# Kernel optimization log

Measured on AMD Instinct MI355X. Metric: run time of the kernel, lower is better.

The kernel has to match this reference:

```python
import jax, jax.numpy as jnp
import numpy as np

B, T, C = 8, 1024, 768
H = 12
HS = C // H  # 64


def setup_inputs() -> dict:
    key = jax.random.key(0)
    ks = jax.random.split(key, 6)
    s = C ** -0.5
    x = jax.random.normal(ks[0], (B, T, C), dtype=jnp.float32)
    Wq = jax.random.normal(ks[1], (H, C, HS), dtype=jnp.float32) * s
    Wk = jax.random.normal(ks[2], (H, C, HS), dtype=jnp.float32) * s
    Wv = jax.random.normal(ks[3], (H, C, HS), dtype=jnp.float32) * s
    Wproj = jax.random.normal(ks[4], (C, C), dtype=jnp.float32) * s
    bproj = jax.random.normal(ks[5], (C,), dtype=jnp.float32) * 0.01
    return {"x": x, "Wq": Wq, "Wk": Wk, "Wv": Wv, "Wproj": Wproj, "bproj": bproj}


def reference(x, Wq, Wk, Wv, Wproj, bproj):
    # per-head projections (equivalent to stacked per-head nn.Linear, bias=False)
    q = jnp.einsum('btc,hcd->bhtd', x, Wq)
    k = jnp.einsum('btc,hcd->bhtd', x, Wk)
    v = jnp.einsum('btc,hcd->bhtd', x, Wv)
    scale = HS ** -0.5
    scores = jnp.einsum('bhtd,bhsd->bhts', q, k) * scale  # [B,H,T,T]
    causal = jnp.tril(jnp.ones((T, T), dtype=bool))
    scores = jnp.where(causal, scores, -jnp.inf)
    weights = jax.nn.softmax(scores, axis=-1)
    out = jnp.einsum('bhts,bhsd->bhtd', weights, v)  # [B,H,T,HS]
    out = out.transpose(0, 2, 1, 3).reshape(B, T, C)  # concat heads
    # output projection (dropout is identity in eval mode)
    return out @ Wproj.T + bproj
```

## Files before the change

kernel.cpp:

```cpp
#include <hip/hip_runtime.h>


typedef short bf16x8 __attribute__((ext_vector_type(8)));
typedef float f32x4 __attribute__((ext_vector_type(4)));

static __device__ __forceinline__ unsigned short f2bf(float f) {
  unsigned int u = __float_as_uint(f);
  u += 0x7fffu + ((u >> 16) & 1u);
  return (unsigned short)(u >> 16);
}

static __device__ __forceinline__ void gl_lds16(const void* g, void* l) {
  __builtin_amdgcn_global_load_lds(
      (const __attribute__((address_space(1))) unsigned int*)g,
      (__attribute__((address_space(3))) unsigned int*)l, 16, 0, 0);
}

__global__ void k_cast4(const float* __restrict__ src, unsigned short* __restrict__ dst, int n4) {
  int i = blockIdx.x * 256 + threadIdx.x;
  if (i < n4) {
    float4 f = ((const float4*)src)[i];
    ushort4 o;
    o.x = f2bf(f.x); o.y = f2bf(f.y); o.z = f2bf(f.z); o.w = f2bf(f.w);
    ((ushort4*)dst)[i] = o;
  }
}

__global__ __launch_bounds__(256) void k_prep_w(const float* __restrict__ Wq,
                                                const float* __restrict__ Wk,
                                                const float* __restrict__ Wv,
                                                unsigned short* __restrict__ wt) {
  __shared__ float tb[64][65];
  const int c0 = blockIdx.x * 64;
  const int hq = blockIdx.y;
  const int qi = hq / 12, h = hq % 12;
  const float* W = (qi == 0) ? Wq : ((qi == 1) ? Wk : Wv);
  const int tid = threadIdx.x;
  {
    int rowb = tid >> 4;
    int col4 = (tid & 15) * 4;
#pragma unroll
    for (int it = 0; it < 4; ++it) {
      int c = it * 16 + rowb;
      float4 f = *(const float4*)(W + (h * 768 + c0 + c) * 64 + col4);
      tb[c][col4] = f.x; tb[c][col4 + 1] = f.y; tb[c][col4 + 2] = f.z; tb[c][col4 + 3] = f.w;
    }
  }
  __syncthreads();
#pragma unroll
  for (int it = 0; it < 2; ++it) {
    int slot = it * 256 + tid;
    int d = slot >> 3, cg = (slot & 7) * 8;
    union { unsigned short a[8]; uint4 v; } o;
#pragma unroll
    for (int j = 0; j < 8; ++j) o.a[j] = f2bf(tb[cg + j][d]);
    *(uint4*)(wt + (qi * 768 + h * 64 + d) * 768 + c0 + cg) = o.v;
  }
}

__global__ __launch_bounds__(256) void k_gemm_qkv(
    const unsigned short* __restrict__ xb,
    const unsigned short* __restrict__ wt,
    unsigned short* __restrict__ qkv) {
  __shared__ unsigned short As[128 * 32];
  __shared__ unsigned short Bs[128 * 32];
  const int tid = threadIdx.x;
  const int w = tid >> 6, lane = tid & 63, quad = lane >> 4, lr = lane & 15;
  const int wm = w >> 1, wn = w & 1;
  const int m0 = blockIdx.x * 128, n0 = blockIdx.y * 128;

  f32x4 acc[4][4] = {};

  const int srow = w * 16 + (lane >> 2);
  const int scol = (lane & 3) * 8;
  const unsigned short* ga0 = xb + (m0 + srow) * 768 + scol;
  const unsigned short* ga1 = ga0 + 64 * 768;
  const unsigned short* gb0 = wt + (n0 + srow) * 768 + scol;
  const unsigned short* gb1 = gb0 + 64 * 768;
  unsigned short* la0 = &As[(w * 16) * 32];
  unsigned short* la1 = la0 + 64 * 32;
  unsigned short* lb0 = &Bs[(w * 16) * 32];
  unsigned short* lb1 = lb0 + 64 * 32;

  for (int k0 = 0; k0 < 768; k0 += 32) {
    gl_lds16(ga0 + k0, la0);
    gl_lds16(ga1 + k0, la1);
    gl_lds16(gb0 + k0, lb0);
    gl_lds16(gb1 + k0, lb1);
    __syncthreads();
    bf16x8 af[4], bfr[4];
#pragma unroll
    for (int i = 0; i < 4; ++i)
      af[i] = *(const bf16x8*)(&As[(wm * 64 + i * 16 + lr) * 32 + quad * 8]);
#pragma unroll
    for (int j = 0; j < 4; ++j)
      bfr[j] = *(const bf16x8*)(&Bs[(wn * 64 + j * 16 + lr) * 32 + quad * 8]);
#pragma unroll
    for (int i = 0; i < 4; ++i)
#pragma unroll
      for (int j = 0; j < 4; ++j)
        acc[i][j] = __builtin_amdgcn_mfma_f32_16x16x32_bf16(af[i], bfr[j], acc[i][j], 0, 0, 0);
    __syncthreads();
  }

#pragma unroll
  for (int j = 0; j < 4; ++j) {
    int n = n0 + wn * 64 + j * 16 + lr;
    int qi = n / 768;
    int rr = n - qi * 768;
    int h = rr >> 6, d = rr & 63;
#pragma unroll
    for (int i = 0; i < 4; ++i) {
#pragma unroll
      for (int r = 0; r < 4; ++r) {
        int m = m0 + wm * 64 + i * 16 + quad * 4 + r;
        int b = m >> 10, t = m & 1023;
        qkv[(((qi * 8 + b) * 12 + h) * 1024 + t) * 64 + d] = f2bf(acc[i][j][r]);
      }
    }
  }
}

__global__ __launch_bounds__(256) void k_transV(const unsigned short* __restrict__ Vn,
                                                unsigned short* __restrict__ Vt) {
  __shared__ unsigned short tb[64][80];
  const int t0 = blockIdx.x * 64;
  const int bh = blockIdx.y;
  const unsigned short* src = Vn + bh * 65536;
  unsigned short* dst = Vt + bh * 65536;
  const int tid = threadIdx.x;
#pragma unroll
  for (int p = 0; p < 2; ++p) {
    int idx = p * 256 + tid;
    int row = idx >> 3, c8 = idx & 7;
    *(uint4*)&tb[row][c8 * 8] = *(const uint4*)(src + (t0 + row) * 64 + c8 * 8);
  }
  __syncthreads();
  int d = tid >> 2, tq = (tid & 3) * 16;
  unsigned short tmp[16];
#pragma unroll
  for (int k = 0; k < 16; ++k) tmp[k] = tb[tq + k][d];
  *(uint4*)(dst + d * 1024 + t0 + tq) = *(uint4*)&tmp[0];
  *(uint4*)(dst + d * 1024 + t0 + tq + 8) = *(uint4*)&tmp[8];
}

__global__ __launch_bounds__(256) void k_attn(
    const unsigned short* __restrict__ qkv,
    const unsigned short* __restrict__ Vtg,
    unsigned short* __restrict__ attn) {
  __shared__ unsigned short Kbuf[2][64 * 64];
  __shared__ unsigned short Vbuf[2][64 * 64];
  __shared__ unsigned short Pbuf[4][32 * 72];
  const int tid = threadIdx.x;
  const int w = tid >> 6, lane = tid & 63, quad = lane >> 4, lr = lane & 15;
  const int hb = blockIdx.x;
  const int qb = 7 - (int)blockIdx.y;
  const int h = hb % 12, b = hb / 12;
  const int HT = 65536;
  const unsigned short* Q  = qkv + (b * 12 + h) * HT;
  const unsigned short* K  = qkv + (96 + b * 12 + h) * HT;
  const unsigned short* Vt = Vtg + (b * 12 + h) * HT;

  bf16x8 aq[2][2];
#pragma unroll
  for (int i = 0; i < 2; ++i)
#pragma unroll
    for (int hf = 0; hf < 2; ++hf)
      aq[i][hf] = *(const bf16x8*)(Q + (qb * 128 + w * 32 + i * 16 + lr) * 64 + hf * 32 + quad * 8);

  f32x4 accO[2][4] = {};
  float lsum[2][4] = {};

  const int nc = 2 * qb + 2;
  const float c1 = 0.125f * 1.4426950408889634f;
  const float c0 = -4.0f * 1.4426950408889634f;

  auto stage = [&](int bi, int sc) {
#pragma unroll
    for (int j = 0; j < 2; ++j) {
      int row = w * 16 + j * 8 + (lane >> 3);
      int c8 = (lane & 7) ^ (row & 7);
      gl_lds16(K + (sc * 64 + row) * 64 + c8 * 8, &Kbuf[bi][(w * 16 + j * 8) * 64]);
      gl_lds16(Vt + row * 1024 + sc * 64 + c8 * 8, &Vbuf[bi][(w * 16 + j * 8) * 64]);
    }
  };

  stage(0, 0);
  for (int sc = 0; sc < nc; ++sc) {
    __syncthreads();
    if (sc + 1 < nc) stage((sc + 1) & 1, sc + 1);
    const unsigned short* Kl = Kbuf[sc & 1];
    const unsigned short* Vl = Vbuf[sc & 1];

    f32x4 accS[2][4];
#pragma unroll
    for (int i = 0; i < 2; ++i)
#pragma unroll
      for (int nt = 0; nt < 4; ++nt) {
        f32x4 z = {};
#pragma unroll
        for (int hf = 0; hf < 2; ++hf) {
          int s = nt * 16 + lr;
          bf16x8 kb = *(const bf16x8*)(Kl + (s * 8 + ((4 * hf + quad) ^ (s & 7))) * 8);
          z = __builtin_amdgcn_mfma_f32_16x16x32_bf16(aq[i][hf], kb, z, 0, 0, 0);
        }
        accS[i][nt] = z;
      }

#pragma unroll
    for (int i = 0; i < 2; ++i) {
      const int base_i = qb * 128 + w * 32 + i * 16;
      const bool needmask = (sc * 64 + 63 > base_i);
#pragma unroll
      for (int r = 0; r < 4; ++r) {
        int tg = base_i + quad * 4 + r;
#pragma unroll
        for (int nt = 0; nt < 4; ++nt) {
          float p = __builtin_amdgcn_exp2f(fmaf(accS[i][nt][r], c1, c0));
          if (needmask && (sc * 64 + nt * 16 + lr > tg)) p = 0.f;
          lsum[i][r] += p;
          Pbuf[w][(i * 16 + quad * 4 + r) * 72 + nt * 16 + lr] = f2bf(p);
        }
      }
    }

#pragma unroll
    for (int i = 0; i < 2; ++i) {
      bf16x8 pa[2];
#pragma unroll
      for (int hf = 0; hf < 2; ++hf)
        pa[hf] = *(const bf16x8*)(&Pbuf[w][(i * 16 + lr) * 72 + hf * 32 + quad * 8]);
#pragma unroll
      for (int ntd = 0; ntd < 4; ++ntd) {
        int d = ntd * 16 + lr;
#pragma unroll
        for (int hf = 0; hf < 2; ++hf) {
          bf16x8 vb = *(const bf16x8*)(Vl + (d * 8 + ((4 * hf + quad) ^ (d & 7))) * 8);
          accO[i][ntd] = __builtin_amdgcn_mfma_f32_16x16x32_bf16(pa[hf], vb, accO[i][ntd], 0, 0, 0);
        }
      }
    }
  }

  float linv[2][4];
#pragma unroll
  for (int i = 0; i < 2; ++i)
#pragma unroll
    for (int r = 0; r < 4; ++r) {
      float l = lsum[i][r];
      l += __shfl_xor(l, 1);
      l += __shfl_xor(l, 2);
      l += __shfl_xor(l, 4);
      l += __shfl_xor(l, 8);
      linv[i][r] = 1.0f / l;
    }

#pragma unroll
  for (int i = 0; i < 2; ++i)
#pragma unroll
    for (int ntd = 0; ntd < 4; ++ntd) {
      int c = h * 64 + ntd * 16 + lr;
#pragma unroll
      for (int r = 0; r < 4; ++r) {
        int t = qb * 128 + w * 32 + i * 16 + quad * 4 + r;
        attn[(b * 1024 + t) * 768 + c] = f2bf(accO[i][ntd][r] * linv[i][r]);
      }
    }
}

__global__ __launch_bounds__(256) void k_gemm_proj(
    const unsigned short* __restrict__ ab,
    const unsigned short* __restrict__ wp,
    const float* __restrict__ bias,
    float* __restrict__ out) {
  __shared__ unsigned short As[128 * 32];
  __shared__ unsigned short Bs[128 * 32];
  const int tid = threadIdx.x;
  const int w = tid >> 6, lane = tid & 63, quad = lane >> 4, lr = lane & 15;
  const int wm = w >> 1, wn = w & 1;
  const int m0 = blockIdx.x * 128, n0 = blockIdx.y * 128;

  f32x4 acc[4][4] = {};

  const int srow = w * 16 + (lane >> 2);
  const int scol = (lane & 3) * 8;
  const unsigned short* ga0 = ab + (m0 + srow) * 768 + scol;
  const unsigned short* ga1 = ga0 + 64 * 768;
  const unsigned short* gb0 = wp + (n0 + srow) * 768 + scol;
  const unsigned short* gb1 = gb0 + 64 * 768;
  unsigned short* la0 = &As[(w * 16) * 32];
  unsigned short* la1 = la0 + 64 * 32;
  unsigned short* lb0 = &Bs[(w * 16) * 32];
  unsigned short* lb1 = lb0 + 64 * 32;

  for (int k0 = 0; k0 < 768; k0 += 32) {
    gl_lds16(ga0 + k0, la0);
    gl_lds16(ga1 + k0, la1);
    gl_lds16(gb0 + k0, lb0);
    gl_lds16(gb1 + k0, lb1);
    __syncthreads();
    bf16x8 af[4], bfr[4];
#pragma unroll
    for (int i = 0; i < 4; ++i)
      af[i] = *(const bf16x8*)(&As[(wm * 64 + i * 16 + lr) * 32 + quad * 8]);
#pragma unroll
    for (int j = 0; j < 4; ++j)
      bfr[j] = *(const bf16x8*)(&Bs[(wn * 64 + j * 16 + lr) * 32 + quad * 8]);
#pragma unroll
    for (int i = 0; i < 4; ++i)
#pragma unroll
      for (int j = 0; j < 4; ++j)
        acc[i][j] = __builtin_amdgcn_mfma_f32_16x16x32_bf16(af[i], bfr[j], acc[i][j], 0, 0, 0);
    __syncthreads();
  }

#pragma unroll
  for (int j = 0; j < 4; ++j) {
    int ncol = n0 + wn * 64 + j * 16 + lr;
    float bv = bias[ncol];
#pragma unroll
    for (int i = 0; i < 4; ++i) {
#pragma unroll
      for (int r = 0; r < 4; ++r) {
        int m = m0 + wm * 64 + i * 16 + quad * 4 + r;
        out[m * 768 + ncol] = acc[i][j][r] + bv;
      }
    }
  }
}

extern "C" void kernel_launch(void* const* d_in, const int* in_sizes, int n_in,
                              void* d_out, int out_size, void* d_ws, size_t ws_size,
                              hipStream_t stream) {
  const float* x     = (const float*)d_in[0];
  const float* Wq    = (const float*)d_in[1];
  const float* Wk    = (const float*)d_in[2];
  const float* Wv    = (const float*)d_in[3];
  const float* Wproj = (const float*)d_in[4];
  const float* bproj = (const float*)d_in[5];
  float* out = (float*)d_out;

  char* p = (char*)d_ws;
  unsigned short* xb   = (unsigned short*)p; p += 12582912;
  unsigned short* wt   = (unsigned short*)p; p += 3538944;
  unsigned short* wp   = (unsigned short*)p; p += 1179648;
  unsigned short* qkv  = (unsigned short*)p; p += 37748736;
  unsigned short* attn = (unsigned short*)p; p += 12582912;
  unsigned short* Vt   = xb;
  const unsigned short* Vn = qkv + 2 * 96 * 65536;

  k_cast4<<<6144, 256, 0, stream>>>(x, xb, 8192 * 768 / 4);
  k_cast4<<<576, 256, 0, stream>>>(Wproj, wp, 768 * 768 / 4);
  k_prep_w<<<dim3(12, 36), 256, 0, stream>>>(Wq, Wk, Wv, wt);
  k_gemm_qkv<<<dim3(64, 18), 256, 0, stream>>>(xb, wt, qkv);
  k_transV<<<dim3(16, 96), 256, 0, stream>>>(Vn, Vt);
  k_attn<<<dim3(96, 8), 256, 0, stream>>>(qkv, Vt, attn);
  k_gemm_proj<<<dim3(64, 6), 256, 0, stream>>>(attn, wp, bproj, out);
}
```

Baseline: 196.7 us.

## Fuse prep kernels, write V transposed from QKV GEMM, stage epilogues through LDS

The three cast/prep launches are merged into a single kernel indexed by block id. The QKV GEMM now stages its output tile in shared memory and writes Q/K rows, and V already transposed, with 16-byte stores, which removes the separate V transpose kernel and its extra global round trip. The projection GEMM epilogue also goes through LDS so that bias add and fp32 stores become coalesced float4 writes. The cost is extra LDS traffic and barriers in the epilogues, plus higher LDS use from the union buffers.

```diff
diff --git a/kernel.cpp b/kernel.cpp
--- a/kernel.cpp
+++ b/kernel.cpp
@@ -16,26 +16,30 @@
       (__attribute__((address_space(3))) unsigned int*)l, 16, 0, 0);
 }
 
-__global__ void k_cast4(const float* __restrict__ src, unsigned short* __restrict__ dst, int n4) {
-  int i = blockIdx.x * 256 + threadIdx.x;
-  if (i < n4) {
+__global__ __launch_bounds__(256) void k_prep(
+    const float* __restrict__ x, const float* __restrict__ Wproj,
+    const float* __restrict__ Wq, const float* __restrict__ Wk,
+    const float* __restrict__ Wv,
+    unsigned short* __restrict__ xb, unsigned short* __restrict__ wp,
+    unsigned short* __restrict__ wt) {
+  __shared__ float tb[64][65];
+  const int bx = blockIdx.x;
+  const int tid = threadIdx.x;
+  if (bx < 6720) {
+    const float* src = (bx < 6144) ? x : Wproj;
+    unsigned short* dst = (bx < 6144) ? xb : wp;
+    int i = (bx < 6144 ? bx : bx - 6144) * 256 + tid;
     float4 f = ((const float4*)src)[i];
     ushort4 o;
     o.x = f2bf(f.x); o.y = f2bf(f.y); o.z = f2bf(f.z); o.w = f2bf(f.w);
     ((ushort4*)dst)[i] = o;
-  }
-}
-
-__global__ __launch_bounds__(256) void k_prep_w(const float* __restrict__ Wq,
-                                                const float* __restrict__ Wk,
-                                                const float* __restrict__ Wv,
-                                                unsigned short* __restrict__ wt) {
-  __shared__ float tb[64][65];
-  const int c0 = blockIdx.x * 64;
-  const int hq = blockIdx.y;
+    return;
+  }
+  const int idx = bx - 6720;
+  const int c0 = (idx % 12) * 64;
+  const int hq = idx / 12;
   const int qi = hq / 12, h = hq % 12;
   const float* W = (qi == 0) ? Wq : ((qi == 1) ? Wk : Wv);
-  const int tid = threadIdx.x;
   {
     int rowb = tid >> 4;
     int col4 = (tid & 15) * 4;
@@ -61,9 +65,12 @@
 __global__ __launch_bounds__(256) void k_gemm_qkv(
     const unsigned short* __restrict__ xb,
     const unsigned short* __restrict__ wt,
-    unsigned short* __restrict__ qkv) {
-  __shared__ unsigned short As[128 * 32];
-  __shared__ unsigned short Bs[128 * 32];
+    unsigned short* __restrict__ qkv,
+    unsigned short* __restrict__ vt) {
+  __shared__ union {
+    unsigned short ab[2][128 * 32];
+    unsigned short c[128][132];
+  } sm;
   const int tid = threadIdx.x;
   const int w = tid >> 6, lane = tid & 63, quad = lane >> 4, lr = lane & 15;
   const int wm = w >> 1, wn = w & 1;
@@ -77,9 +84,11 @@
   const unsigned short* ga1 = ga0 + 64 * 768;
   const unsigned short* gb0 = wt + (n0 + srow) * 768 + scol;
   const unsigned short* gb1 = gb0 + 64 * 768;
-  unsigned short* la0 = &As[(w * 16) * 32];
+  unsigned short* As = sm.ab[0];
+  unsigned short* Bs = sm.ab[1];
+  unsigned short* la0 = As + (w * 16) * 32;
   unsigned short* la1 = la0 + 64 * 32;
-  unsigned short* lb0 = &Bs[(w * 16) * 32];
+  unsigned short* lb0 = Bs + (w * 16) * 32;
   unsigned short* lb1 = lb0 + 64 * 32;
 
   for (int k0 = 0; k0 < 768; k0 += 32) {
@@ -104,44 +113,36 @@
   }
 
 #pragma unroll
-  for (int j = 0; j < 4; ++j) {
-    int n = n0 + wn * 64 + j * 16 + lr;
-    int qi = n / 768;
-    int rr = n - qi * 768;
-    int h = rr >> 6, d = rr & 63;
-#pragma unroll
-    for (int i = 0; i < 4; ++i) {
-#pragma unroll
-      for (int r = 0; r < 4; ++r) {
-        int m = m0 + wm * 64 + i * 16 + quad * 4 + r;
-        int b = m >> 10, t = m & 1023;
-        qkv[(((qi * 8 + b) * 12 + h) * 1024 + t) * 64 + d] = f2bf(acc[i][j][r]);
-      }
-    }
-  }
-}
-
-__global__ __launch_bounds__(256) void k_transV(const unsigned short* __restrict__ Vn,
-                                                unsigned short* __restrict__ Vt) {
-  __shared__ unsigned short tb[64][80];
-  const int t0 = blockIdx.x * 64;
-  const int bh = blockIdx.y;
-  const unsigned short* src = Vn + bh * 65536;
-  unsigned short* dst = Vt + bh * 65536;
-  const int tid = threadIdx.x;
-#pragma unroll
-  for (int p = 0; p < 2; ++p) {
-    int idx = p * 256 + tid;
-    int row = idx >> 3, c8 = idx & 7;
-    *(uint4*)&tb[row][c8 * 8] = *(const uint4*)(src + (t0 + row) * 64 + c8 * 8);
-  }
+  for (int i = 0; i < 4; ++i)
+#pragma unroll
+    for (int j = 0; j < 4; ++j)
+#pragma unroll
+      for (int r = 0; r < 4; ++r)
+        sm.c[wm * 64 + i * 16 + quad * 4 + r][wn * 64 + j * 16 + lr] = f2bf(acc[i][j][r]);
   __syncthreads();
-  int d = tid >> 2, tq = (tid & 3) * 16;
-  unsigned short tmp[16];
-#pragma unroll
-  for (int k = 0; k < 16; ++k) tmp[k] = tb[tq + k][d];
-  *(uint4*)(dst + d * 1024 + t0 + tq) = *(uint4*)&tmp[0];
-  *(uint4*)(dst + d * 1024 + t0 + tq + 8) = *(uint4*)&tmp[8];
+
+  const int qi = n0 / 768;
+  const int rr0 = n0 - qi * 768;
+  const int h0 = rr0 >> 6;
+  const int b = m0 >> 10, t0 = m0 & 1023;
+  if (qi < 2) {
+    int t_local = tid >> 1, hh = tid & 1;
+    unsigned short* dst = qkv + (size_t)(((qi * 8 + b) * 12 + h0 + hh) * 1024 + t0 + t_local) * 64;
+    const unsigned short* src = &sm.c[t_local][hh * 64];
+#pragma unroll
+    for (int k = 0; k < 8; ++k)
+      *(uint4*)(dst + k * 8) = *(const uint4*)(src + k * 8);
+  } else {
+    int hh = tid >> 7, d = (tid >> 1) & 63, th = tid & 1;
+    unsigned short* dst = vt + (size_t)((b * 12 + h0 + hh) * 64 + d) * 1024 + t0 + th * 64;
+#pragma unroll
+    for (int k0 = 0; k0 < 8; ++k0) {
+      union { unsigned short a[8]; uint4 v; } o;
+#pragma unroll
+      for (int kk = 0; kk < 8; ++kk) o.a[kk] = sm.c[th * 64 + k0 * 8 + kk][hh * 64 + d];
+      *(uint4*)(dst + k0 * 8) = o.v;
+    }
+  }
 }
 
 __global__ __launch_bounds__(256) void k_attn(
@@ -273,8 +274,10 @@
     const unsigned short* __restrict__ wp,
     const float* __restrict__ bias,
     float* __restrict__ out) {
-  __shared__ unsigned short As[128 * 32];
-  __shared__ unsigned short Bs[128 * 32];
+  __shared__ union {
+    unsigned short ab2[2][128 * 32];
+    float cf[64][134];
+  } sm;
   const int tid = threadIdx.x;
   const int w = tid >> 6, lane = tid & 63, quad = lane >> 4, lr = lane & 15;
   const int wm = w >> 1, wn = w & 1;
@@ -288,9 +291,11 @@
   const unsigned short* ga1 = ga0 + 64 * 768;
   const unsigned short* gb0 = wp + (n0 + srow) * 768 + scol;
   const unsigned short* gb1 = gb0 + 64 * 768;
-  unsigned short* la0 = &As[(w * 16) * 32];
+  unsigned short* As = sm.ab2[0];
+  unsigned short* Bs = sm.ab2[1];
+  unsigned short* la0 = As + (w * 16) * 32;
   unsigned short* la1 = la0 + 64 * 32;
-  unsigned short* lb0 = &Bs[(w * 16) * 32];
+  unsigned short* lb0 = Bs + (w * 16) * 32;
   unsigned short* lb1 = lb0 + 64 * 32;
 
   for (int k0 = 0; k0 < 768; k0 += 32) {
@@ -315,17 +320,28 @@
   }
 
 #pragma unroll
-  for (int j = 0; j < 4; ++j) {
-    int ncol = n0 + wn * 64 + j * 16 + lr;
-    float bv = bias[ncol];
-#pragma unroll
-    for (int i = 0; i < 4; ++i) {
-#pragma unroll
-      for (int r = 0; r < 4; ++r) {
-        int m = m0 + wm * 64 + i * 16 + quad * 4 + r;
-        out[m * 768 + ncol] = acc[i][j][r] + bv;
-      }
-    }
+  for (int p = 0; p < 2; ++p) {
+    if (wm == p) {
+#pragma unroll
+      for (int i = 0; i < 4; ++i)
+#pragma unroll
+        for (int j = 0; j < 4; ++j)
+#pragma unroll
+          for (int r = 0; r < 4; ++r)
+            sm.cf[i * 16 + quad * 4 + r][wn * 64 + j * 16 + lr] = acc[i][j][r];
+    }
+    __syncthreads();
+    int row = tid >> 2, cq = (tid & 3) * 32;
+    const float* brow = bias + n0 + cq;
+    float* orow = out + (size_t)(m0 + p * 64 + row) * 768 + n0 + cq;
+#pragma unroll
+    for (int k = 0; k < 8; ++k) {
+      float4 v = *(const float4*)&sm.cf[row][cq + k * 4];
+      float4 bv = *(const float4*)(brow + k * 4);
+      v.x += bv.x; v.y += bv.y; v.z += bv.z; v.w += bv.w;
+      *(float4*)(orow + k * 4) = v;
+    }
+    __syncthreads();
   }
 }
 
@@ -346,14 +362,10 @@
   unsigned short* wp   = (unsigned short*)p; p += 1179648;
   unsigned short* qkv  = (unsigned short*)p; p += 37748736;
   unsigned short* attn = (unsigned short*)p; p += 12582912;
-  unsigned short* Vt   = xb;
-  const unsigned short* Vn = qkv + 2 * 96 * 65536;
-
-  k_cast4<<<6144, 256, 0, stream>>>(x, xb, 8192 * 768 / 4);
-  k_cast4<<<576, 256, 0, stream>>>(Wproj, wp, 768 * 768 / 4);
-  k_prep_w<<<dim3(12, 36), 256, 0, stream>>>(Wq, Wk, Wv, wt);
-  k_gemm_qkv<<<dim3(64, 18), 256, 0, stream>>>(xb, wt, qkv);
-  k_transV<<<dim3(16, 96), 256, 0, stream>>>(Vn, Vt);
-  k_attn<<<dim3(96, 8), 256, 0, stream>>>(qkv, Vt, attn);
+  unsigned short* vt   = qkv + (size_t)192 * 65536;
+
+  k_prep<<<7152, 256, 0, stream>>>(x, Wproj, Wq, Wk, Wv, xb, wp, wt);
+  k_gemm_qkv<<<dim3(64, 18), 256, 0, stream>>>(xb, wt, qkv, vt);
+  k_attn<<<dim3(96, 8), 256, 0, stream>>>(qkv, vt, attn);
   k_gemm_proj<<<dim3(64, 6), 256, 0, stream>>>(attn, wp, bproj, out);
 }
```

After: 203.3 us. 3.3% more time.

## Merge prep kernels, pad Pbuf differently, stage proj epilogue through LDS

Applied to the files above, without the earlier changes.

Folds the two cast launches and the weight-transpose launch into a single prep kernel that dispatches on block index, so two kernel launches are removed. The padding of the attention P buffer's row stride changes from 72 to 68 elements to alter the LDS bank mapping. The output-projection epilogue now stages accumulators through shared memory (unioned with the A/B tiles) in two halves and writes coalesced float4 rows with the bias added, replacing scattered scalar stores at the cost of extra barriers and LDS traffic.

```diff
diff --git a/kernel.cpp b/kernel.cpp
--- a/kernel.cpp
+++ b/kernel.cpp
@@ -16,26 +16,30 @@
       (__attribute__((address_space(3))) unsigned int*)l, 16, 0, 0);
 }
 
-__global__ void k_cast4(const float* __restrict__ src, unsigned short* __restrict__ dst, int n4) {
-  int i = blockIdx.x * 256 + threadIdx.x;
-  if (i < n4) {
+__global__ __launch_bounds__(256) void k_prep(
+    const float* __restrict__ x, const float* __restrict__ Wproj,
+    const float* __restrict__ Wq, const float* __restrict__ Wk,
+    const float* __restrict__ Wv,
+    unsigned short* __restrict__ xb, unsigned short* __restrict__ wp,
+    unsigned short* __restrict__ wt) {
+  __shared__ float tb[64][65];
+  const int bx = blockIdx.x;
+  const int tid = threadIdx.x;
+  if (bx < 6720) {
+    const float* src = (bx < 6144) ? x : Wproj;
+    unsigned short* dst = (bx < 6144) ? xb : wp;
+    int i = (bx < 6144 ? bx : bx - 6144) * 256 + tid;
     float4 f = ((const float4*)src)[i];
     ushort4 o;
     o.x = f2bf(f.x); o.y = f2bf(f.y); o.z = f2bf(f.z); o.w = f2bf(f.w);
     ((ushort4*)dst)[i] = o;
-  }
-}
-
-__global__ __launch_bounds__(256) void k_prep_w(const float* __restrict__ Wq,
-                                                const float* __restrict__ Wk,
-                                                const float* __restrict__ Wv,
-                                                unsigned short* __restrict__ wt) {
-  __shared__ float tb[64][65];
-  const int c0 = blockIdx.x * 64;
-  const int hq = blockIdx.y;
+    return;
+  }
+  const int idx = bx - 6720;
+  const int c0 = (idx % 12) * 64;
+  const int hq = idx / 12;
   const int qi = hq / 12, h = hq % 12;
   const float* W = (qi == 0) ? Wq : ((qi == 1) ? Wk : Wv);
-  const int tid = threadIdx.x;
   {
     int rowb = tid >> 4;
     int col4 = (tid & 15) * 4;
@@ -150,7 +154,7 @@
     unsigned short* __restrict__ attn) {
   __shared__ unsigned short Kbuf[2][64 * 64];
   __shared__ unsigned short Vbuf[2][64 * 64];
-  __shared__ unsigned short Pbuf[4][32 * 72];
+  __shared__ unsigned short Pbuf[4][32 * 68];
   const int tid = threadIdx.x;
   const int w = tid >> 6, lane = tid & 63, quad = lane >> 4, lr = lane & 15;
   const int hb = blockIdx.x;
@@ -219,7 +223,7 @@
           float p = __builtin_amdgcn_exp2f(fmaf(accS[i][nt][r], c1, c0));
           if (needmask && (sc * 64 + nt * 16 + lr > tg)) p = 0.f;
           lsum[i][r] += p;
-          Pbuf[w][(i * 16 + quad * 4 + r) * 72 + nt * 16 + lr] = f2bf(p);
+          Pbuf[w][(i * 16 + quad * 4 + r) * 68 + nt * 16 + lr] = f2bf(p);
         }
       }
     }
@@ -229,7 +233,7 @@
       bf16x8 pa[2];
 #pragma unroll
       for (int hf = 0; hf < 2; ++hf)
-        pa[hf] = *(const bf16x8*)(&Pbuf[w][(i * 16 + lr) * 72 + hf * 32 + quad * 8]);
+        pa[hf] = *(const bf16x8*)(&Pbuf[w][(i * 16 + lr) * 68 + hf * 32 + quad * 8]);
 #pragma unroll
       for (int ntd = 0; ntd < 4; ++ntd) {
         int d = ntd * 16 + lr;
@@ -273,8 +277,10 @@
     const unsigned short* __restrict__ wp,
     const float* __restrict__ bias,
     float* __restrict__ out) {
-  __shared__ unsigned short As[128 * 32];
-  __shared__ unsigned short Bs[128 * 32];
+  __shared__ union {
+    unsigned short ab2[2][128 * 32];
+    float cf[64][134];
+  } sm;
   const int tid = threadIdx.x;
   const int w = tid >> 6, lane = tid & 63, quad = lane >> 4, lr = lane & 15;
   const int wm = w >> 1, wn = w & 1;
@@ -288,9 +294,11 @@
   const unsigned short* ga1 = ga0 + 64 * 768;
   const unsigned short* gb0 = wp + (n0 + srow) * 768 + scol;
   const unsigned short* gb1 = gb0 + 64 * 768;
-  unsigned short* la0 = &As[(w * 16) * 32];
+  unsigned short* As = sm.ab2[0];
+  unsigned short* Bs = sm.ab2[1];
+  unsigned short* la0 = As + (w * 16) * 32;
   unsigned short* la1 = la0 + 64 * 32;
-  unsigned short* lb0 = &Bs[(w * 16) * 32];
+  unsigned short* lb0 = Bs + (w * 16) * 32;
   unsigned short* lb1 = lb0 + 64 * 32;
 
   for (int k0 = 0; k0 < 768; k0 += 32) {
@@ -315,17 +323,28 @@
   }
 
 #pragma unroll
-  for (int j = 0; j < 4; ++j) {
-    int ncol = n0 + wn * 64 + j * 16 + lr;
-    float bv = bias[ncol];
-#pragma unroll
-    for (int i = 0; i < 4; ++i) {
-#pragma unroll
-      for (int r = 0; r < 4; ++r) {
-        int m = m0 + wm * 64 + i * 16 + quad * 4 + r;
-        out[m * 768 + ncol] = acc[i][j][r] + bv;
-      }
-    }
+  for (int p = 0; p < 2; ++p) {
+    if (wm == p) {
+#pragma unroll
+      for (int i = 0; i < 4; ++i)
+#pragma unroll
+        for (int j = 0; j < 4; ++j)
+#pragma unroll
+          for (int r = 0; r < 4; ++r)
+            sm.cf[i * 16 + quad * 4 + r][wn * 64 + j * 16 + lr] = acc[i][j][r];
+    }
+    __syncthreads();
+    int row = tid >> 2, cq = (tid & 3) * 32;
+    const float* brow = bias + n0 + cq;
+    float* orow = out + (size_t)(m0 + p * 64 + row) * 768 + n0 + cq;
+#pragma unroll
+    for (int k = 0; k < 8; ++k) {
+      float4 v = *(const float4*)&sm.cf[row][cq + k * 4];
+      float4 bv = *(const float4*)(brow + k * 4);
+      v.x += bv.x; v.y += bv.y; v.z += bv.z; v.w += bv.w;
+      *(float4*)(orow + k * 4) = v;
+    }
+    __syncthreads();
   }
 }
 
@@ -347,11 +366,9 @@
   unsigned short* qkv  = (unsigned short*)p; p += 37748736;
   unsigned short* attn = (unsigned short*)p; p += 12582912;
   unsigned short* Vt   = xb;
-  const unsigned short* Vn = qkv + 2 * 96 * 65536;
-
-  k_cast4<<<6144, 256, 0, stream>>>(x, xb, 8192 * 768 / 4);
-  k_cast4<<<576, 256, 0, stream>>>(Wproj, wp, 768 * 768 / 4);
-  k_prep_w<<<dim3(12, 36), 256, 0, stream>>>(Wq, Wk, Wv, wt);
+  const unsigned short* Vn = qkv + (size_t)192 * 65536;
+
+  k_prep<<<7152, 256, 0, stream>>>(x, Wproj, Wq, Wk, Wv, xb, wp, wt);
   k_gemm_qkv<<<dim3(64, 18), 256, 0, stream>>>(xb, wt, qkv);
   k_transV<<<dim3(16, 96), 256, 0, stream>>>(Vn, Vt);
   k_attn<<<dim3(96, 8), 256, 0, stream>>>(qkv, Vt, attn);
```

New measurement: 204.4 us. 3.9% more time.

## Fuse prep kernels and write V transposed directly from QKV GEMM epilogue

Applied to the files above, without the earlier changes.

Merges the x cast, Wproj cast and QKV weight transpose into one launch with block-index dispatch. The QKV GEMM epilogue now writes V straight into a transposed [b,h,d,t] layout with 8-byte stores, so the separate V transpose kernel and its extra read/write pass over V are gone. The attention P buffer row stride is also changed from 72 to 68 to alter LDS bank mapping. Risks include less coalesced V stores and possible bank or alignment effects from the new P stride.

```diff
diff --git a/kernel.cpp b/kernel.cpp
--- a/kernel.cpp
+++ b/kernel.cpp
@@ -16,26 +16,30 @@
       (__attribute__((address_space(3))) unsigned int*)l, 16, 0, 0);
 }
 
-__global__ void k_cast4(const float* __restrict__ src, unsigned short* __restrict__ dst, int n4) {
-  int i = blockIdx.x * 256 + threadIdx.x;
-  if (i < n4) {
+__global__ __launch_bounds__(256) void k_prep(
+    const float* __restrict__ x, const float* __restrict__ Wproj,
+    const float* __restrict__ Wq, const float* __restrict__ Wk,
+    const float* __restrict__ Wv,
+    unsigned short* __restrict__ xb, unsigned short* __restrict__ wp,
+    unsigned short* __restrict__ wt) {
+  __shared__ float tb[64][65];
+  const int bx = blockIdx.x;
+  const int tid = threadIdx.x;
+  if (bx < 6720) {
+    const float* src = (bx < 6144) ? x : Wproj;
+    unsigned short* dst = (bx < 6144) ? xb : wp;
+    int i = (bx < 6144 ? bx : bx - 6144) * 256 + tid;
     float4 f = ((const float4*)src)[i];
     ushort4 o;
     o.x = f2bf(f.x); o.y = f2bf(f.y); o.z = f2bf(f.z); o.w = f2bf(f.w);
     ((ushort4*)dst)[i] = o;
-  }
-}
-
-__global__ __launch_bounds__(256) void k_prep_w(const float* __restrict__ Wq,
-                                                const float* __restrict__ Wk,
-                                                const float* __restrict__ Wv,
-                                                unsigned short* __restrict__ wt) {
-  __shared__ float tb[64][65];
-  const int c0 = blockIdx.x * 64;
-  const int hq = blockIdx.y;
+    return;
+  }
+  const int idx = bx - 6720;
+  const int c0 = (idx % 12) * 64;
+  const int hq = idx / 12;
   const int qi = hq / 12, h = hq % 12;
   const float* W = (qi == 0) ? Wq : ((qi == 1) ? Wk : Wv);
-  const int tid = threadIdx.x;
   {
     int rowb = tid >> 4;
     int col4 = (tid & 15) * 4;
@@ -61,7 +65,8 @@
 __global__ __launch_bounds__(256) void k_gemm_qkv(
     const unsigned short* __restrict__ xb,
     const unsigned short* __restrict__ wt,
-    unsigned short* __restrict__ qkv) {
+    unsigned short* __restrict__ qkv,
+    unsigned short* __restrict__ vt) {
   __shared__ unsigned short As[128 * 32];
   __shared__ unsigned short Bs[128 * 32];
   const int tid = threadIdx.x;
@@ -103,45 +108,38 @@
     __syncthreads();
   }
 
-#pragma unroll
-  for (int j = 0; j < 4; ++j) {
-    int n = n0 + wn * 64 + j * 16 + lr;
-    int qi = n / 768;
-    int rr = n - qi * 768;
-    int h = rr >> 6, d = rr & 63;
-#pragma unroll
-    for (int i = 0; i < 4; ++i) {
-#pragma unroll
-      for (int r = 0; r < 4; ++r) {
-        int m = m0 + wm * 64 + i * 16 + quad * 4 + r;
-        int b = m >> 10, t = m & 1023;
-        qkv[(((qi * 8 + b) * 12 + h) * 1024 + t) * 64 + d] = f2bf(acc[i][j][r]);
-      }
-    }
-  }
-}
-
-__global__ __launch_bounds__(256) void k_transV(const unsigned short* __restrict__ Vn,
-                                                unsigned short* __restrict__ Vt) {
-  __shared__ unsigned short tb[64][80];
-  const int t0 = blockIdx.x * 64;
-  const int bh = blockIdx.y;
-  const unsigned short* src = Vn + bh * 65536;
-  unsigned short* dst = Vt + bh * 65536;
-  const int tid = threadIdx.x;
-#pragma unroll
-  for (int p = 0; p < 2; ++p) {
-    int idx = p * 256 + tid;
-    int row = idx >> 3, c8 = idx & 7;
-    *(uint4*)&tb[row][c8 * 8] = *(const uint4*)(src + (t0 + row) * 64 + c8 * 8);
-  }
-  __syncthreads();
-  int d = tid >> 2, tq = (tid & 3) * 16;
-  unsigned short tmp[16];
-#pragma unroll
-  for (int k = 0; k < 16; ++k) tmp[k] = tb[tq + k][d];
-  *(uint4*)(dst + d * 1024 + t0 + tq) = *(uint4*)&tmp[0];
-  *(uint4*)(dst + d * 1024 + t0 + tq + 8) = *(uint4*)&tmp[8];
+  const int qi = n0 / 768;
+  const int b = m0 >> 10, t0 = m0 & 1023;
+  if (qi < 2) {
+#pragma unroll
+    for (int j = 0; j < 4; ++j) {
+      int rr = (n0 - qi * 768) + wn * 64 + j * 16 + lr;
+      int h = rr >> 6, d = rr & 63;
+#pragma unroll
+      for (int i = 0; i < 4; ++i) {
+#pragma unroll
+        for (int r = 0; r < 4; ++r) {
+          int t = t0 + wm * 64 + i * 16 + quad * 4 + r;
+          qkv[(size_t)(((qi * 8 + b) * 12 + h) * 1024 + t) * 64 + d] = f2bf(acc[i][j][r]);
+        }
+      }
+    }
+  } else {
+#pragma unroll
+    for (int j = 0; j < 4; ++j) {
+      int rr = (n0 - 1536) + wn * 64 + j * 16 + lr;
+      int h = rr >> 6, d = rr & 63;
+      unsigned short* vrow = vt + (size_t)((b * 12 + h) * 64 + d) * 1024;
+#pragma unroll
+      for (int i = 0; i < 4; ++i) {
+        int t = t0 + wm * 64 + i * 16 + quad * 4;
+        union { unsigned short a[4]; unsigned int u[2]; } o;
+#pragma unroll
+        for (int r = 0; r < 4; ++r) o.a[r] = f2bf(acc[i][j][r]);
+        *(uint2*)(vrow + t) = *(uint2*)&o.u[0];
+      }
+    }
+  }
 }
 
 __global__ __launch_bounds__(256) void k_attn(
@@ -150,7 +148,7 @@
     unsigned short* __restrict__ attn) {
   __shared__ unsigned short Kbuf[2][64 * 64];
   __shared__ unsigned short Vbuf[2][64 * 64];
-  __shared__ unsigned short Pbuf[4][32 * 72];
+  __shared__ unsigned short Pbuf[4][32 * 68];
   const int tid = threadIdx.x;
   const int w = tid >> 6, lane = tid & 63, quad = lane >> 4, lr = lane & 15;
   const int hb = blockIdx.x;
@@ -219,7 +217,7 @@
           float p = __builtin_amdgcn_exp2f(fmaf(accS[i][nt][r], c1, c0));
           if (needmask && (sc * 64 + nt * 16 + lr > tg)) p = 0.f;
           lsum[i][r] += p;
-          Pbuf[w][(i * 16 + quad * 4 + r) * 72 + nt * 16 + lr] = f2bf(p);
+          Pbuf[w][(i * 16 + quad * 4 + r) * 68 + nt * 16 + lr] = f2bf(p);
         }
       }
     }
@@ -229,7 +227,7 @@
       bf16x8 pa[2];
 #pragma unroll
       for (int hf = 0; hf < 2; ++hf)
-        pa[hf] = *(const bf16x8*)(&Pbuf[w][(i * 16 + lr) * 72 + hf * 32 + quad * 8]);
+        pa[hf] = *(const bf16x8*)(&Pbuf[w][(i * 16 + lr) * 68 + hf * 32 + quad * 8]);
 #pragma unroll
       for (int ntd = 0; ntd < 4; ++ntd) {
         int d = ntd * 16 + lr;
@@ -323,7 +321,7 @@
 #pragma unroll
       for (int r = 0; r < 4; ++r) {
         int m = m0 + wm * 64 + i * 16 + quad * 4 + r;
-        out[m * 768 + ncol] = acc[i][j][r] + bv;
+        out[(size_t)m * 768 + ncol] = acc[i][j][r] + bv;
       }
     }
   }
@@ -346,14 +344,10 @@
   unsigned short* wp   = (unsigned short*)p; p += 1179648;
   unsigned short* qkv  = (unsigned short*)p; p += 37748736;
   unsigned short* attn = (unsigned short*)p; p += 12582912;
-  unsigned short* Vt   = xb;
-  const unsigned short* Vn = qkv + 2 * 96 * 65536;
-
-  k_cast4<<<6144, 256, 0, stream>>>(x, xb, 8192 * 768 / 4);
-  k_cast4<<<576, 256, 0, stream>>>(Wproj, wp, 768 * 768 / 4);
-  k_prep_w<<<dim3(12, 36), 256, 0, stream>>>(Wq, Wk, Wv, wt);
-  k_gemm_qkv<<<dim3(64, 18), 256, 0, stream>>>(xb, wt, qkv);
-  k_transV<<<dim3(16, 96), 256, 0, stream>>>(Vn, Vt);
-  k_attn<<<dim3(96, 8), 256, 0, stream>>>(qkv, Vt, attn);
+  unsigned short* vt   = qkv + (size_t)192 * 65536;
+
+  k_prep<<<7152, 256, 0, stream>>>(x, Wproj, Wq, Wk, Wv, xb, wp, wt);
+  k_gemm_qkv<<<dim3(64, 18), 256, 0, stream>>>(xb, wt, qkv, vt);
+  k_attn<<<dim3(96, 8), 256, 0, stream>>>(qkv, vt, attn);
   k_gemm_proj<<<dim3(64, 6), 256, 0, stream>>>(attn, wp, bproj, out);
 }
```

After: 201.8 us. 2.6% more time.
